# Optimization experiments

Measured on AMD Instinct MI355X. Metric: run time of the kernel, lower is better.

The kernel has to match this reference:

```python
import jax, jax.numpy as jnp
import numpy as np

B, S, HID = 4, 2048, 2048
NH, NKV, HD = 16, 4, 128  # head_dim = HID // NH
Q_SIZE, KV_SIZE = NH * HD, NKV * HD


def setup_inputs() -> dict:
    key = jax.random.key(0)
    ks = jax.random.split(key, 8)
    pos = jnp.arange(S, dtype=jnp.float32)[:, None]
    inv_freq = 1.0 / (10000.0 ** (jnp.arange(0, HD, 2, dtype=jnp.float32) / HD))  # [HD/2]
    ang = pos * inv_freq[None, :]  # [S, HD/2]
    return {
        "hidden_states": jax.random.normal(ks[0], (B, S, HID), jnp.float32),
        "rotary_pos_emb_cos": jnp.cos(ang),
        "rotary_pos_emb_sin": jnp.sin(ang),
        "w_qkv": jax.random.normal(ks[1], (HID, Q_SIZE + 2 * KV_SIZE), jnp.float32) * (HID ** -0.5),
        "b_qkv": jax.random.normal(ks[2], (Q_SIZE + 2 * KV_SIZE,), jnp.float32) * 0.02,
        "w_o": jax.random.normal(ks[3], (HID, HID), jnp.float32) * (HID ** -0.5),
        "b_o": jax.random.normal(ks[4], (HID,), jnp.float32) * 0.02,
    }


def _apply_rope(x, cos, sin):
    # x: [B, S, H, D]; cos/sin: [S, D/2]; rotate-half (non-interleaved) convention
    d2 = x.shape[-1] // 2
    x1, x2 = x[..., :d2], x[..., d2:]
    c = cos[None, :, None, :]
    s = sin[None, :, None, :]
    return jnp.concatenate([x1 * c - x2 * s, x2 * c + x1 * s], axis=-1)


def reference(hidden_states, rotary_pos_emb_cos, rotary_pos_emb_sin, w_qkv, b_qkv, w_o, b_o):
    b, s, _ = hidden_states.shape
    qkv = hidden_states @ w_qkv + b_qkv  # [B, S, Q_SIZE + 2*KV_SIZE]
    q, k, v = jnp.split(qkv, [Q_SIZE, Q_SIZE + KV_SIZE], axis=-1)
    q = q.reshape(b, s, NH, HD)
    k = k.reshape(b, s, NKV, HD)
    v = v.reshape(b, s, NKV, HD)
    q = _apply_rope(q, rotary_pos_emb_cos, rotary_pos_emb_sin)
    k = _apply_rope(k, rotary_pos_emb_cos, rotary_pos_emb_sin)
    # grouped-query attention: repeat kv heads to match query heads
    g = NH // NKV
    k = jnp.repeat(k, g, axis=2)  # [B, S, NH, HD]
    v = jnp.repeat(v, g, axis=2)
    scale = HD ** -0.5
    scores = jnp.einsum("bshd,bthd->bhst", q, k) * scale  # [B, NH, S, S]
    probs = jax.nn.softmax(scores, axis=-1)
    out = jnp.einsum("bhst,bthd->bshd", probs, v)  # [B, S, NH, HD]
    out = out.reshape(b, s, NH * HD)
    return out @ w_o + b_o
```

## Files before the change

kernel.cpp:

```cpp
#include <hip/hip_runtime.h>
#include <math.h>

#define B_N   4
#define S_N   2048
#define HID_N 2048
#define NH_N  16
#define NKV_N 4
#define HD_N  128
#define QSZ   2048
#define KVSZ  512
#define QKVN  3072
#define M_N   8192

typedef __bf16 bf16;
typedef __bf16 bf16x8 __attribute__((ext_vector_type(8)));
typedef float  f32x4  __attribute__((ext_vector_type(4)));

#define GLL16(gp, lp)                                                          \
  __builtin_amdgcn_global_load_lds(                                            \
      (const __attribute__((address_space(1))) void*)(gp),                     \
      (__attribute__((address_space(3))) void*)(lp), 16, 0, 0)

__device__ __forceinline__ f32x4 mfma16(bf16x8 a, bf16x8 b, f32x4 c) {
  return __builtin_amdgcn_mfma_f32_16x16x32_bf16(a, b, c, 0, 0, 0);
}

__global__ __launch_bounds__(256) void conv_bf16_kernel(
    const float* __restrict__ X, bf16* __restrict__ Y)
{
  size_t i = ((size_t)blockIdx.x * 256 + threadIdx.x) * 8;
  float4 a = *(const float4*)&X[i];
  float4 b = *(const float4*)&X[i + 4];
  union { bf16 h[8]; uint4 u; } pk;
  pk.h[0] = (bf16)a.x; pk.h[1] = (bf16)a.y; pk.h[2] = (bf16)a.z; pk.h[3] = (bf16)a.w;
  pk.h[4] = (bf16)b.x; pk.h[5] = (bf16)b.y; pk.h[6] = (bf16)b.z; pk.h[7] = (bf16)b.w;
  *(uint4*)&Y[i] = pk.u;
}

__global__ __launch_bounds__(256) void convT_kernel(
    const float* __restrict__ W, bf16* __restrict__ Wt, int K, int N)
{
  __shared__ __attribute__((aligned(16))) bf16 tile[64 * 68];
  const int n0 = blockIdx.x * 64, k0 = blockIdx.y * 64;
#pragma unroll
  for (int it = 0; it < 4; ++it) {
    int idx = it * 256 + threadIdx.x;
    int r = idx >> 4, c4 = (idx & 15) << 2;
    float4 v = *(const float4*)&W[(size_t)(k0 + r) * N + n0 + c4];
    union { bf16 h[4]; unsigned long long u; } pk;
    pk.h[0] = (bf16)v.x; pk.h[1] = (bf16)v.y; pk.h[2] = (bf16)v.z; pk.h[3] = (bf16)v.w;
    *(unsigned long long*)&tile[r * 68 + c4] = pk.u;
  }
  __syncthreads();
#pragma unroll
  for (int it = 0; it < 4; ++it) {
    int idx = it * 256 + threadIdx.x;
    int rn = idx >> 4, ck4 = (idx & 15) << 2;
    union { bf16 h[4]; unsigned long long u; } pk;
#pragma unroll
    for (int i = 0; i < 4; ++i) pk.h[i] = tile[(ck4 + i) * 68 + rn];
    *(unsigned long long*)&Wt[(size_t)(n0 + rn) * K + k0 + ck4] = pk.u;
  }
}

template <bool OUT_BF16>
__global__ __launch_bounds__(256, 2) void gemm_bf16_kernel(
    const bf16* __restrict__ A, const bf16* __restrict__ Bt,
    const float* __restrict__ bias, void* __restrict__ Cout,
    int M, int N, int K)
{
  __shared__ __attribute__((aligned(16))) bf16 As[128 * 32];
  __shared__ __attribute__((aligned(16))) bf16 Bs[128 * 32];

  const int tid  = threadIdx.x;
  const int lane = tid & 63, wv = tid >> 6;
  const int quad = lane >> 4, ln = lane & 15;
  const int row0 = blockIdx.y * 128, col0 = blockIdx.x * 128;
  const int wr = (wv >> 1) * 64, wc = (wv & 1) * 64;

  f32x4 acc[4][4];
  const f32x4 zero = {0.f, 0.f, 0.f, 0.f};
#pragma unroll
  for (int mt = 0; mt < 4; ++mt)
#pragma unroll
    for (int nt = 0; nt < 4; ++nt) acc[mt][nt] = zero;

  const int s0 = wv * 128 + lane;
  const bf16* gA0 = A  + (size_t)(row0 + (s0 >> 2)) * K + (s0 & 3) * 8;
  const bf16* gA1 = gA0 + 16 * (size_t)K;
  const bf16* gB0 = Bt + (size_t)(col0 + (s0 >> 2)) * K + (s0 & 3) * 8;
  const bf16* gB1 = gB0 + 16 * (size_t)K;
  bf16* lA0 = As + (size_t)wv * 1024;
  bf16* lA1 = lA0 + 512;
  bf16* lB0 = Bs + (size_t)wv * 1024;
  bf16* lB1 = lB0 + 512;

  for (int k0 = 0; k0 < K; k0 += 32) {
    GLL16(gA0 + k0, lA0);
    GLL16(gA1 + k0, lA1);
    GLL16(gB0 + k0, lB0);
    GLL16(gB1 + k0, lB1);
    __syncthreads();

    bf16x8 a[4], b[4];
#pragma unroll
    for (int mt = 0; mt < 4; ++mt)
      a[mt] = *(const bf16x8*)&As[(wr + mt * 16 + ln) * 32 + quad * 8];
#pragma unroll
    for (int nt = 0; nt < 4; ++nt)
      b[nt] = *(const bf16x8*)&Bs[(wc + nt * 16 + ln) * 32 + quad * 8];
#pragma unroll
    for (int mt = 0; mt < 4; ++mt)
#pragma unroll
      for (int nt = 0; nt < 4; ++nt)
        acc[mt][nt] = mfma16(a[mt], b[nt], acc[mt][nt]);
    __syncthreads();
  }

#pragma unroll
  for (int nt = 0; nt < 4; ++nt) {
    const int c = col0 + wc + nt * 16 + ln;
    const float bv = bias[c];
#pragma unroll
    for (int mt = 0; mt < 4; ++mt) {
#pragma unroll
      for (int r = 0; r < 4; ++r) {
        const int rr = row0 + wr + mt * 16 + quad * 4 + r;
        const float v = acc[mt][nt][r] + bv;
        if (OUT_BF16) ((bf16*)Cout)[(size_t)rr * N + c] = (bf16)v;
        else          ((float*)Cout)[(size_t)rr * N + c] = v;
      }
    }
  }
}

__global__ __launch_bounds__(256) void rope_repack_kernel(
    const bf16* __restrict__ qkvB, const float* __restrict__ cosb,
    const float* __restrict__ sinb, bf16* __restrict__ Qb, bf16* __restrict__ Kb)
{
  int idx = blockIdx.x * 256 + threadIdx.x;
  int j  = idx & 63;
  int m  = (idx >> 6) & (M_N - 1);
  int hh = idx >> 19;
  int b = m >> 11, s = m & (S_N - 1);
  float c  = cosb[s * 64 + j];
  float sn = sinb[s * 64 + j];
  if (hh < NH_N) {
    const bf16* src = qkvB + (size_t)m * QKVN + hh * HD_N;
    float x1 = (float)src[j], x2 = (float)src[j + 64];
    bf16* dst = Qb + ((size_t)(b * NH_N + hh) * S_N + s) * HD_N;
    const float qs = 0.08838834764831845f * 1.4426950408889634f;
    dst[j]      = (bf16)((x1 * c - x2 * sn) * qs);
    dst[j + 64] = (bf16)((x2 * c + x1 * sn) * qs);
  } else {
    int kh = hh - NH_N;
    const bf16* src = qkvB + (size_t)m * QKVN + QSZ + kh * HD_N;
    float x1 = (float)src[j], x2 = (float)src[j + 64];
    bf16* dst = Kb + ((size_t)(b * NKV_N + kh) * S_N + s) * HD_N;
    dst[j]      = (bf16)(x1 * c - x2 * sn);
    dst[j + 64] = (bf16)(x2 * c + x1 * sn);
  }
}

__global__ __launch_bounds__(256) void transposeV_kernel(
    const bf16* __restrict__ qkvB, bf16* __restrict__ Vt)
{
  __shared__ __attribute__((aligned(16))) bf16 tile[64 * 136];
  const int s0 = blockIdx.x * 64;
  const int bkh = blockIdx.y;
  const int b = bkh >> 2, kh = bkh & 3;
#pragma unroll
  for (int it = 0; it < 4; ++it) {
    int ci = it * 256 + threadIdx.x;
    int r = ci >> 4, c = ci & 15;
    uint4 v = *(const uint4*)&qkvB[(size_t)(b * S_N + s0 + r) * QKVN +
                                   QSZ + KVSZ + kh * HD_N + c * 8];
    *(uint4*)&tile[r * 136 + c * 8] = v;
  }
  __syncthreads();
#pragma unroll
  for (int it = 0; it < 4; ++it) {
    int ci = it * 256 + threadIdx.x;
    int d = ci >> 3, c = ci & 7;
    union { bf16 h[8]; uint4 u; } pk;
#pragma unroll
    for (int i = 0; i < 8; ++i) pk.h[i] = tile[(c * 8 + i) * 136 + d];
    *(uint4*)&Vt[((size_t)bkh * HD_N + d) * S_N + s0 + c * 8] = pk.u;
  }
}

__global__ __launch_bounds__(256, 3) void attn_mfma_kernel(
    const bf16* __restrict__ Qb, const bf16* __restrict__ Kb,
    const bf16* __restrict__ Vt, bf16* __restrict__ Ob)
{
  __shared__ __attribute__((aligned(16))) bf16 Ks[64 * 128];
  __shared__ __attribute__((aligned(16))) bf16 Vs[128 * 64];
  __shared__ __attribute__((aligned(16))) bf16 Ps[128 * 72];

  const int tid  = threadIdx.x;
  const int lane = tid & 63, wv = tid >> 6;
  const int quad = lane >> 4, ln = lane & 15;
  const int q0 = blockIdx.x * 128;
  const int h  = blockIdx.y, b = blockIdx.z;
  const int kh = h >> 2;

  const bf16* Qg = Qb + ((size_t)(b * NH_N + h) * S_N + q0) * HD_N;
  const bf16* Kg = Kb + (size_t)(b * NKV_N + kh) * S_N * HD_N;
  const bf16* Vg = Vt + (size_t)(b * NKV_N + kh) * HD_N * S_N;

  bf16x8 aq[2][4];
#pragma unroll
  for (int g = 0; g < 2; ++g) {
    const bf16* qrow = Qg + (size_t)((wv * 2 + g) * 16 + ln) * HD_N;
#pragma unroll
    for (int dc = 0; dc < 4; ++dc)
      aq[g][dc] = *(const bf16x8*)&qrow[(dc * 4 + quad) * 8];
  }

  bf16x8 bones;
#pragma unroll
  for (int j = 0; j < 8; ++j) bones[j] = (ln == 0) ? (bf16)1.0f : (bf16)0.0f;

  f32x4 accO[2][8];
  const f32x4 zero = {0.f, 0.f, 0.f, 0.f};
#pragma unroll
  for (int g = 0; g < 2; ++g)
#pragma unroll
    for (int dt = 0; dt < 8; ++dt) accO[g][dt] = zero;
  f32x4 accL[2] = {zero, zero};

  for (int kt = 0; kt < S_N; kt += 64) {
#pragma unroll
    for (int t = 0; t < 4; ++t) {
      int slot = (t * 4 + wv) * 64 + lane;
      int row = slot >> 4, cc = slot & 15;
      int csrc = (cc & 8) | ((cc & 7) ^ (row & 7));
      GLL16(Kg + (size_t)(kt + row) * 128 + csrc * 8,
            Ks + (size_t)(t * 4 + wv) * 512);
    }
#pragma unroll
    for (int t = 0; t < 4; ++t) {
      int slot = (t * 4 + wv) * 64 + lane;
      int row = slot >> 3, cc = slot & 7;
      int csrc = cc ^ (row & 7);
      GLL16(Vg + (size_t)row * S_N + kt + csrc * 8,
            Vs + (size_t)(t * 4 + wv) * 512);
    }
    __syncthreads();

    f32x4 accS[2][4];
#pragma unroll
    for (int g = 0; g < 2; ++g)
#pragma unroll
      for (int nt = 0; nt < 4; ++nt) accS[g][nt] = zero;
#pragma unroll
    for (int nt = 0; nt < 4; ++nt) {
      const int kp = nt * 16 + ln;
#pragma unroll
      for (int dc = 0; dc < 4; ++dc) {
        int c = dc * 4 + quad;
        int cs = (c & 8) | ((c & 7) ^ (kp & 7));
        bf16x8 bk = *(const bf16x8*)&Ks[kp * 128 + cs * 8];
        accS[0][nt] = mfma16(aq[0][dc], bk, accS[0][nt]);
        accS[1][nt] = mfma16(aq[1][dc], bk, accS[1][nt]);
      }
    }

#pragma unroll
    for (int g = 0; g < 2; ++g)
#pragma unroll
      for (int r = 0; r < 4; ++r) {
        const int q = (wv * 2 + g) * 16 + quad * 4 + r;
        bf16* pr = &Ps[q * 72 + ln];
        pr[0]  = (bf16)__builtin_amdgcn_exp2f(accS[g][0][r]);
        pr[16] = (bf16)__builtin_amdgcn_exp2f(accS[g][1][r]);
        pr[32] = (bf16)__builtin_amdgcn_exp2f(accS[g][2][r]);
        pr[48] = (bf16)__builtin_amdgcn_exp2f(accS[g][3][r]);
      }

    bf16x8 ap0[2], ap1[2];
#pragma unroll
    for (int g = 0; g < 2; ++g) {
      const int qr = ((wv * 2 + g) * 16 + ln) * 72;
      ap0[g] = *(const bf16x8*)&Ps[qr + quad * 8];
      ap1[g] = *(const bf16x8*)&Ps[qr + 32 + quad * 8];
      accL[g] = mfma16(ap0[g], bones, accL[g]);
      accL[g] = mfma16(ap1[g], bones, accL[g]);
    }
#pragma unroll
    for (int dt = 0; dt < 8; ++dt) {
      const int d = dt * 16 + ln;
      {
        int cs = quad ^ (d & 7);
        bf16x8 bv = *(const bf16x8*)&Vs[d * 64 + cs * 8];
        accO[0][dt] = mfma16(ap0[0], bv, accO[0][dt]);
        accO[1][dt] = mfma16(ap0[1], bv, accO[1][dt]);
      }
      {
        int cs = (4 + quad) ^ (d & 7);
        bf16x8 bv = *(const bf16x8*)&Vs[d * 64 + cs * 8];
        accO[0][dt] = mfma16(ap1[0], bv, accO[0][dt]);
        accO[1][dt] = mfma16(ap1[1], bv, accO[1][dt]);
      }
    }
    __syncthreads();
  }

#pragma unroll
  for (int g = 0; g < 2; ++g)
#pragma unroll
    for (int r = 0; r < 4; ++r) {
      const float l = __shfl(accL[g][r], lane & 48);
      const float inv = 1.f / l;
      const int q = q0 + (wv * 2 + g) * 16 + quad * 4 + r;
      const size_t base = ((size_t)b * S_N + q) * HID_N + h * HD_N;
#pragma unroll
      for (int dt = 0; dt < 8; ++dt)
        Ob[base + dt * 16 + ln] = (bf16)(accO[g][dt][r] * inv);
    }
}

extern "C" void kernel_launch(void* const* d_in, const int* in_sizes, int n_in,
                              void* d_out, int out_size, void* d_ws, size_t ws_size,
                              hipStream_t stream) {
  const float* hidden = (const float*)d_in[0];
  const float* cosb   = (const float*)d_in[1];
  const float* sinb   = (const float*)d_in[2];
  const float* w_qkv  = (const float*)d_in[3];
  const float* b_qkv  = (const float*)d_in[4];
  const float* w_o    = (const float*)d_in[5];
  const float* b_o    = (const float*)d_in[6];
  float* out = (float*)d_out;

  char* w = (char*)d_ws;
  bf16* qkvB  = (bf16*)(w);
  bf16* Qb    = (bf16*)(w + 50331648);
  bf16* Kb    = (bf16*)(w + 83886080);
  bf16* Vt    = (bf16*)(w + 92274688);
  bf16* wqkvT = (bf16*)(w + 100663296);
  bf16* woT   = (bf16*)(w + 113246208);
  bf16* hidB  = (bf16*)(w + 121634816);
  bf16* attnB = hidB;

  conv_bf16_kernel<<<(M_N * HID_N) / (256 * 8), 256, 0, stream>>>(hidden, hidB);
  convT_kernel<<<dim3(QKVN / 64, HID_N / 64), 256, 0, stream>>>(w_qkv, wqkvT, HID_N, QKVN);
  convT_kernel<<<dim3(HID_N / 64, HID_N / 64), 256, 0, stream>>>(w_o, woT, HID_N, HID_N);

  gemm_bf16_kernel<true><<<dim3(QKVN / 128, M_N / 128), 256, 0, stream>>>(
      hidB, wqkvT, b_qkv, qkvB, M_N, QKVN, HID_N);

  rope_repack_kernel<<<(M_N * (NH_N + NKV_N) * 64) / 256, 256, 0, stream>>>(
      qkvB, cosb, sinb, Qb, Kb);
  transposeV_kernel<<<dim3(S_N / 64, B_N * NKV_N), 256, 0, stream>>>(qkvB, Vt);

  attn_mfma_kernel<<<dim3(S_N / 128, NH_N, B_N), 256, 0, stream>>>(Qb, Kb, Vt, attnB);

  gemm_bf16_kernel<false><<<dim3(HID_N / 128, M_N / 128), 256, 0, stream>>>(
      attnB, woT, b_o, out, M_N, HID_N, HID_N);
}
```

Before: 611.7 us.

## Prefetch next K/V tile into registers and remap attention blocks by XCD

The attention kernel now loads the next K/V tile into registers while the current tile's MFMAs run, then writes it to LDS between barriers. This replaces the per-iteration direct global-to-LDS loads that stalled before compute. The launch also switches to a 1D grid with a swizzled block-to-(batch, kv-head, head, q-tile) mapping, so blocks sharing a KV head land on the same XCD for L2 reuse. The register prefetch adds register pressure at launch_bounds(256,3), and the extra barrier plus register-to-LDS copy add cost per tile.

```diff
diff --git a/kernel.cpp b/kernel.cpp
--- a/kernel.cpp
+++ b/kernel.cpp
@@ -200,9 +200,14 @@
   const int tid  = threadIdx.x;
   const int lane = tid & 63, wv = tid >> 6;
   const int quad = lane >> 4, ln = lane & 15;
-  const int q0 = blockIdx.x * 128;
-  const int h  = blockIdx.y, b = blockIdx.z;
-  const int kh = h >> 2;
+
+  const int gid = blockIdx.x;
+  const int xcd = gid & 7, sl = gid >> 3;
+  const int grp = xcd * 2 + (sl >> 6);
+  const int within = sl & 63;
+  const int b = grp >> 2, kh = grp & 3;
+  const int h = kh * 4 + (within >> 4);
+  const int q0 = (within & 15) * 128;
 
   const bf16* Qg = Qb + ((size_t)(b * NH_N + h) * S_N + q0) * HD_N;
   const bf16* Kg = Kb + (size_t)(b * NKV_N + kh) * S_N * HD_N;
@@ -217,6 +222,28 @@
       aq[g][dc] = *(const bf16x8*)&qrow[(dc * 4 + quad) * 8];
   }
 
+  const bf16* kga[4];
+  const bf16* vga[4];
+  int lsl[4];
+#pragma unroll
+  for (int t = 0; t < 4; ++t) {
+    int slot = (t * 4 + wv) * 64 + lane;
+    int row = slot >> 4, cc = slot & 15;
+    int csrc = (cc & 8) | ((cc & 7) ^ (row & 7));
+    kga[t] = Kg + (size_t)row * 128 + csrc * 8;
+    int rowv = slot >> 3, ccv = slot & 7;
+    int csv = ccv ^ (rowv & 7);
+    vga[t] = Vg + (size_t)rowv * S_N + csv * 8;
+    lsl[t] = (t * 4 + wv) * 512 + lane * 8;
+  }
+
+#pragma unroll
+  for (int t = 0; t < 4; ++t)
+    GLL16(kga[t], Ks + (size_t)(t * 4 + wv) * 512);
+#pragma unroll
+  for (int t = 0; t < 4; ++t)
+    GLL16(vga[t], Vs + (size_t)(t * 4 + wv) * 512);
+
   bf16x8 bones;
 #pragma unroll
   for (int j = 0; j < 8; ++j) bones[j] = (ln == 0) ? (bf16)1.0f : (bf16)0.0f;
@@ -229,24 +256,22 @@
     for (int dt = 0; dt < 8; ++dt) accO[g][dt] = zero;
   f32x4 accL[2] = {zero, zero};
 
+  __syncthreads();
+
+  uint4 kr0, kr1, kr2, kr3, vr0, vr1, vr2, vr3;
+
   for (int kt = 0; kt < S_N; kt += 64) {
-#pragma unroll
-    for (int t = 0; t < 4; ++t) {
-      int slot = (t * 4 + wv) * 64 + lane;
-      int row = slot >> 4, cc = slot & 15;
-      int csrc = (cc & 8) | ((cc & 7) ^ (row & 7));
-      GLL16(Kg + (size_t)(kt + row) * 128 + csrc * 8,
-            Ks + (size_t)(t * 4 + wv) * 512);
-    }
-#pragma unroll
-    for (int t = 0; t < 4; ++t) {
-      int slot = (t * 4 + wv) * 64 + lane;
-      int row = slot >> 3, cc = slot & 7;
-      int csrc = cc ^ (row & 7);
-      GLL16(Vg + (size_t)row * S_N + kt + csrc * 8,
-            Vs + (size_t)(t * 4 + wv) * 512);
-    }
-    __syncthreads();
+    const int nkt = kt + 64;
+    if (nkt < S_N) {
+      kr0 = *(const uint4*)(kga[0] + (size_t)nkt * 128);
+      kr1 = *(const uint4*)(kga[1] + (size_t)nkt * 128);
+      kr2 = *(const uint4*)(kga[2] + (size_t)nkt * 128);
+      kr3 = *(const uint4*)(kga[3] + (size_t)nkt * 128);
+      vr0 = *(const uint4*)(vga[0] + nkt);
+      vr1 = *(const uint4*)(vga[1] + nkt);
+      vr2 = *(const uint4*)(vga[2] + nkt);
+      vr3 = *(const uint4*)(vga[3] + nkt);
+    }
 
     f32x4 accS[2][4];
 #pragma unroll
@@ -303,7 +328,19 @@
         accO[1][dt] = mfma16(ap1[1], bv, accO[1][dt]);
       }
     }
-    __syncthreads();
+
+    if (nkt < S_N) {
+      __syncthreads();
+      *(uint4*)&Ks[lsl[0]] = kr0;
+      *(uint4*)&Ks[lsl[1]] = kr1;
+      *(uint4*)&Ks[lsl[2]] = kr2;
+      *(uint4*)&Ks[lsl[3]] = kr3;
+      *(uint4*)&Vs[lsl[0]] = vr0;
+      *(uint4*)&Vs[lsl[1]] = vr1;
+      *(uint4*)&Vs[lsl[2]] = vr2;
+      *(uint4*)&Vs[lsl[3]] = vr3;
+      __syncthreads();
+    }
   }
 
 #pragma unroll
@@ -353,7 +390,7 @@
       qkvB, cosb, sinb, Qb, Kb);
   transposeV_kernel<<<dim3(S_N / 64, B_N * NKV_N), 256, 0, stream>>>(qkvB, Vt);
 
-  attn_mfma_kernel<<<dim3(S_N / 128, NH_N, B_N), 256, 0, stream>>>(Qb, Kb, Vt, attnB);
+  attn_mfma_kernel<<<1024, 256, 0, stream>>>(Qb, Kb, Vt, attnB);
 
   gemm_bf16_kernel<false><<<dim3(HID_N / 128, M_N / 128), 256, 0, stream>>>(
       attnB, woT, b_o, out, M_N, HID_N, HID_N);
```

Measured after the change: 942.8 us. 1.54x slower.

## Double-buffer K/V tiles in attention and remap blocks for XCD-local KV reuse

Applied to the files above, without the earlier changes.

The attention kernel now streams K and V in 32-key tiles into two shared-memory buffers, issuing the async global-to-LDS loads for the next tile before computing on the current one. This hides load latency behind MFMA work. The launch becomes a flat 1D grid whose block index is decoded so that blocks sharing a (batch, kv-head) group land on the same XCD, which should improve L2 reuse of K/V. Halving the tile width doubles the number of loop iterations and barriers, and the loads are only separated from compute by the barrier at the end of each step.

```diff
diff --git a/kernel.cpp b/kernel.cpp
--- a/kernel.cpp
+++ b/kernel.cpp
@@ -193,16 +193,21 @@
     const bf16* __restrict__ Qb, const bf16* __restrict__ Kb,
     const bf16* __restrict__ Vt, bf16* __restrict__ Ob)
 {
-  __shared__ __attribute__((aligned(16))) bf16 Ks[64 * 128];
-  __shared__ __attribute__((aligned(16))) bf16 Vs[128 * 64];
-  __shared__ __attribute__((aligned(16))) bf16 Ps[128 * 72];
+  __shared__ __attribute__((aligned(16))) bf16 Ks[2][32 * 128];
+  __shared__ __attribute__((aligned(16))) bf16 Vs[2][128 * 32];
+  __shared__ __attribute__((aligned(16))) bf16 Ps[128 * 40];
 
   const int tid  = threadIdx.x;
   const int lane = tid & 63, wv = tid >> 6;
   const int quad = lane >> 4, ln = lane & 15;
-  const int q0 = blockIdx.x * 128;
-  const int h  = blockIdx.y, b = blockIdx.z;
-  const int kh = h >> 2;
+
+  const int gid = blockIdx.x;
+  const int xcd = gid & 7, sl = gid >> 3;
+  const int grp = xcd * 2 + (sl >> 6);
+  const int within = sl & 63;
+  const int b = grp >> 2, kh = grp & 3;
+  const int h = kh * 4 + (within >> 4);
+  const int q0 = (within & 15) * 128;
 
   const bf16* Qg = Qb + ((size_t)(b * NH_N + h) * S_N + q0) * HD_N;
   const bf16* Kg = Kb + (size_t)(b * NKV_N + kh) * S_N * HD_N;
@@ -217,6 +222,24 @@
       aq[g][dc] = *(const bf16x8*)&qrow[(dc * 4 + quad) * 8];
   }
 
+  const bf16* kga[2];
+  const bf16* vga[2];
+#pragma unroll
+  for (int t = 0; t < 2; ++t) {
+    int slot = (t * 4 + wv) * 64 + lane;
+    int row = slot >> 4, cc = slot & 15;
+    int csrc = (cc & 8) | ((cc & 7) ^ (row & 7));
+    kga[t] = Kg + (size_t)row * 128 + csrc * 8;
+    int dv = slot >> 2, ccv = slot & 3;
+    int csv = ccv ^ (dv & 3);
+    vga[t] = Vg + (size_t)dv * S_N + csv * 8;
+  }
+
+#pragma unroll
+  for (int t = 0; t < 2; ++t) GLL16(kga[t], &Ks[0][(t * 4 + wv) * 512]);
+#pragma unroll
+  for (int t = 0; t < 2; ++t) GLL16(vga[t], &Vs[0][(t * 4 + wv) * 512]);
+
   bf16x8 bones;
 #pragma unroll
   for (int j = 0; j < 8; ++j) bones[j] = (ln == 0) ? (bf16)1.0f : (bf16)0.0f;
@@ -229,38 +252,35 @@
     for (int dt = 0; dt < 8; ++dt) accO[g][dt] = zero;
   f32x4 accL[2] = {zero, zero};
 
-  for (int kt = 0; kt < S_N; kt += 64) {
-#pragma unroll
-    for (int t = 0; t < 4; ++t) {
-      int slot = (t * 4 + wv) * 64 + lane;
-      int row = slot >> 4, cc = slot & 15;
-      int csrc = (cc & 8) | ((cc & 7) ^ (row & 7));
-      GLL16(Kg + (size_t)(kt + row) * 128 + csrc * 8,
-            Ks + (size_t)(t * 4 + wv) * 512);
-    }
-#pragma unroll
-    for (int t = 0; t < 4; ++t) {
-      int slot = (t * 4 + wv) * 64 + lane;
-      int row = slot >> 3, cc = slot & 7;
-      int csrc = cc ^ (row & 7);
-      GLL16(Vg + (size_t)row * S_N + kt + csrc * 8,
-            Vs + (size_t)(t * 4 + wv) * 512);
-    }
-    __syncthreads();
-
-    f32x4 accS[2][4];
+  __syncthreads();
+
+  int cur = 0;
+  for (int kt = 0; kt < S_N; kt += 32, cur ^= 1) {
+    const int nkt = kt + 32;
+    if (nkt < S_N) {
+#pragma unroll
+      for (int t = 0; t < 2; ++t)
+        GLL16(kga[t] + (size_t)nkt * 128, &Ks[cur ^ 1][(t * 4 + wv) * 512]);
+#pragma unroll
+      for (int t = 0; t < 2; ++t)
+        GLL16(vga[t] + nkt, &Vs[cur ^ 1][(t * 4 + wv) * 512]);
+    }
+    const bf16* Kc = Ks[cur];
+    const bf16* Vc = Vs[cur];
+
+    f32x4 accS[2][2];
 #pragma unroll
     for (int g = 0; g < 2; ++g)
 #pragma unroll
-      for (int nt = 0; nt < 4; ++nt) accS[g][nt] = zero;
-#pragma unroll
-    for (int nt = 0; nt < 4; ++nt) {
+      for (int nt = 0; nt < 2; ++nt) accS[g][nt] = zero;
+#pragma unroll
+    for (int nt = 0; nt < 2; ++nt) {
       const int kp = nt * 16 + ln;
 #pragma unroll
       for (int dc = 0; dc < 4; ++dc) {
         int c = dc * 4 + quad;
         int cs = (c & 8) | ((c & 7) ^ (kp & 7));
-        bf16x8 bk = *(const bf16x8*)&Ks[kp * 128 + cs * 8];
+        bf16x8 bk = *(const bf16x8*)&Kc[kp * 128 + cs * 8];
         accS[0][nt] = mfma16(aq[0][dc], bk, accS[0][nt]);
         accS[1][nt] = mfma16(aq[1][dc], bk, accS[1][nt]);
       }
@@ -271,38 +291,26 @@
 #pragma unroll
       for (int r = 0; r < 4; ++r) {
         const int q = (wv * 2 + g) * 16 + quad * 4 + r;
-        bf16* pr = &Ps[q * 72 + ln];
+        bf16* pr = &Ps[q * 40 + ln];
         pr[0]  = (bf16)__builtin_amdgcn_exp2f(accS[g][0][r]);
         pr[16] = (bf16)__builtin_amdgcn_exp2f(accS[g][1][r]);
-        pr[32] = (bf16)__builtin_amdgcn_exp2f(accS[g][2][r]);
-        pr[48] = (bf16)__builtin_amdgcn_exp2f(accS[g][3][r]);
       }
 
-    bf16x8 ap0[2], ap1[2];
+    bf16x8 ap[2];
 #pragma unroll
     for (int g = 0; g < 2; ++g) {
-      const int qr = ((wv * 2 + g) * 16 + ln) * 72;
-      ap0[g] = *(const bf16x8*)&Ps[qr + quad * 8];
-      ap1[g] = *(const bf16x8*)&Ps[qr + 32 + quad * 8];
-      accL[g] = mfma16(ap0[g], bones, accL[g]);
-      accL[g] = mfma16(ap1[g], bones, accL[g]);
+      ap[g] = *(const bf16x8*)&Ps[((wv * 2 + g) * 16 + ln) * 40 + quad * 8];
+      accL[g] = mfma16(ap[g], bones, accL[g]);
     }
 #pragma unroll
     for (int dt = 0; dt < 8; ++dt) {
       const int d = dt * 16 + ln;
-      {
-        int cs = quad ^ (d & 7);
-        bf16x8 bv = *(const bf16x8*)&Vs[d * 64 + cs * 8];
-        accO[0][dt] = mfma16(ap0[0], bv, accO[0][dt]);
-        accO[1][dt] = mfma16(ap0[1], bv, accO[1][dt]);
-      }
-      {
-        int cs = (4 + quad) ^ (d & 7);
-        bf16x8 bv = *(const bf16x8*)&Vs[d * 64 + cs * 8];
-        accO[0][dt] = mfma16(ap1[0], bv, accO[0][dt]);
-        accO[1][dt] = mfma16(ap1[1], bv, accO[1][dt]);
-      }
-    }
+      int cs = quad ^ (d & 3);
+      bf16x8 bv = *(const bf16x8*)&Vc[d * 32 + cs * 8];
+      accO[0][dt] = mfma16(ap[0], bv, accO[0][dt]);
+      accO[1][dt] = mfma16(ap[1], bv, accO[1][dt]);
+    }
+
     __syncthreads();
   }
 
@@ -353,7 +361,7 @@
       qkvB, cosb, sinb, Qb, Kb);
   transposeV_kernel<<<dim3(S_N / 64, B_N * NKV_N), 256, 0, stream>>>(qkvB, Vt);
 
-  attn_mfma_kernel<<<dim3(S_N / 128, NH_N, B_N), 256, 0, stream>>>(Qb, Kb, Vt, attnB);
+  attn_mfma_kernel<<<1024, 256, 0, stream>>>(Qb, Kb, Vt, attnB);
 
   gemm_bf16_kernel<false><<<dim3(HID_N / 128, M_N / 128), 256, 0, stream>>>(
       attnB, woT, b_o, out, M_N, HID_N, HID_N);
```

After: 548.4 us. 10.4% less time.
